# Optimization experiments

Measured on AMD Instinct MI355X. Metric: run time of the kernel, lower is better.

## Reference

```python
import jax, jax.numpy as jnp
import numpy as np

TEMPERATURE = 0.1
THRESHOLD = 0.5


def setup_inputs() -> dict:
    key = jax.random.key(0)
    k1, k2 = jax.random.split(key)
    B, D, F = 4096, 512, 128
    embeddings = jax.random.normal(k1, (B, D), dtype=jnp.float32)
    similarity_features = jax.random.normal(k2, (B, F), dtype=jnp.float32)
    return {"embeddings": embeddings, "similarity_features": similarity_features}


def reference(embeddings, similarity_features):
    B = embeddings.shape[0]
    # L2-normalize similarity features (F.normalize, eps=1e-12)
    norm = jnp.linalg.norm(similarity_features, axis=1, keepdims=True)
    f = similarity_features / jnp.maximum(norm, 1e-12)
    target_similarity = f @ f.T                                    # [B,B]
    S = (embeddings @ embeddings.T) / TEMPERATURE                  # [B,B] logits

    eye = jnp.eye(B, dtype=bool)
    offdiag = ~eye
    pos = (target_similarity > THRESHOLD) & offdiag
    neg = offdiag & ~pos

    # Per row i: logits = cat(pos_scores, neg_scores) covers ALL off-diagonal
    # entries (len = B-1), labels = 1 on positives, 0 on negatives. Mean BCE:
    #   (1/(B-1)) * sum_{j!=i} [ softplus(-S_ij) if pos else softplus(S_ij) ]
    bce = jnp.where(pos, jax.nn.softplus(-S), jax.nn.softplus(S))
    row_loss = jnp.sum(jnp.where(offdiag, bce, 0.0), axis=1) / jnp.float32(B - 1)

    # Row counted only if it has >=1 positive AND >=1 negative off-diagonal
    valid = (pos.sum(axis=1) > 0) & (neg.sum(axis=1) > 0)
    num_valid = jnp.maximum(valid.sum(), 1).astype(row_loss.dtype)
    loss = jnp.sum(jnp.where(valid, row_loss, 0.0)) / num_valid
    return loss
```

## Files before the change

kernel.cpp:

```cpp
#include <hip/hip_runtime.h>
#include <math.h>


constexpr int Bn = 4096;
constexpr int Dd = 512;
constexpr int Ff = 128;
constexpr float MARGIN = 0.015625f;

typedef __attribute__((ext_vector_type(8))) short bf16x8;
typedef __attribute__((ext_vector_type(4))) float f32x4;

__device__ __forceinline__ ushort f32_to_bf16(float x) {
    unsigned u = __float_as_uint(x);
    unsigned r = (u + 0x7FFFu + ((u >> 16) & 1u)) >> 16;
    return (ushort)r;
}
__device__ __forceinline__ float bf16_to_f32(ushort h) {
    return __uint_as_float(((unsigned)h) << 16);
}

__global__ __launch_bounds__(256) void prep_kernel(const float* __restrict__ sf,
                                                   ushort* __restrict__ fh,
                                                   ushort* __restrict__ fl,
                                                   float* __restrict__ row_sum,
                                                   int* __restrict__ pos_cnt) {
    int gid = blockIdx.x * 256 + threadIdx.x;
    if (gid < Bn) { row_sum[gid] = 0.0f; pos_cnt[gid] = 0; }

    int row = blockIdx.x * 4 + (threadIdx.x >> 6);
    int lane = threadIdx.x & 63;
    const float2 v = *reinterpret_cast<const float2*>(&sf[(size_t)row * Ff + lane * 2]);
    float ss = v.x * v.x + v.y * v.y;
    #pragma unroll
    for (int off = 32; off; off >>= 1) ss += __shfl_xor(ss, off, 64);
    float inv = 1.0f / fmaxf(sqrtf(ss), 1e-12f);
    float fx = v.x * inv, fy = v.y * inv;
    ushort hx = f32_to_bf16(fx), hy = f32_to_bf16(fy);
    ushort lx = f32_to_bf16(fx - bf16_to_f32(hx));
    ushort ly = f32_to_bf16(fy - bf16_to_f32(hy));
    ushort2 h; h.x = hx; h.y = hy;
    ushort2 l; l.x = lx; l.y = ly;
    *reinterpret_cast<ushort2*>(&fh[(size_t)row * Ff + lane * 2]) = h;
    *reinterpret_cast<ushort2*>(&fl[(size_t)row * Ff + lane * 2]) = l;
}

__device__ __forceinline__ void tri_decode(int p, int& bi, int& bj) {
    bi = (int)((sqrtf(8.0f * (float)p + 1.0f) - 1.0f) * 0.5f);
    while ((bi + 1) * (bi + 2) / 2 <= p) ++bi;
    while (bi * (bi + 1) / 2 > p) --bi;
    bj = p - bi * (bi + 1) / 2;
}

__device__ __forceinline__ void stage_tile(const ushort* __restrict__ src, int stride,
                                           int k0, char* tile, int wave, int lane) {
    #pragma unroll
    for (int q = 0; q < 4; ++q) {
        int boff = wave * 4096 + q * 1024 + lane * 16;
        int row = boff >> 7;
        int cb = (boff & 127) ^ ((row & 7) << 4);
        const ushort* g = src + (size_t)row * stride + k0 + (cb >> 1);
        __builtin_amdgcn_global_load_lds(
            (const __attribute__((address_space(1))) void*)g,
            (__attribute__((address_space(3))) void*)(tile + wave * 4096 + q * 1024),
            16, 0, 0);
    }
}

__device__ __forceinline__ void mfma_step(f32x4 (&acc)[4][4], const char* At, const char* Bt,
                                          int wrow, int wcol, int lane) {
    #pragma unroll
    for (int ks = 0; ks < 2; ++ks) {
        bf16x8 a[4], b[4];
        int koff = ks * 64 + ((lane >> 4) << 4);
        #pragma unroll
        for (int m = 0; m < 4; ++m) {
            int row = wrow + m * 16 + (lane & 15);
            a[m] = *reinterpret_cast<const bf16x8*>(At + row * 128 + (koff ^ ((row & 7) << 4)));
        }
        #pragma unroll
        for (int n = 0; n < 4; ++n) {
            int row = wcol + n * 16 + (lane & 15);
            b[n] = *reinterpret_cast<const bf16x8*>(Bt + row * 128 + (koff ^ ((row & 7) << 4)));
        }
        #pragma unroll
        for (int m = 0; m < 4; ++m)
            #pragma unroll
            for (int n = 0; n < 4; ++n)
                acc[m][n] = __builtin_amdgcn_mfma_f32_16x16x32_bf16(a[m], b[n], acc[m][n], 0, 0, 0);
    }
}

__global__ __launch_bounds__(256) void t_kernel(const ushort* __restrict__ Fh,
                                                const ushort* __restrict__ Fl,
                                                unsigned long long* __restrict__ posbits,
                                                int* __restrict__ pos_cnt) {
    __shared__ __align__(16) char smem[32768];
    __shared__ int nf;
    char* At = smem;
    char* Bt = smem + 16384;

    int bi, bj; tri_decode(blockIdx.x, bi, bj);
    const int ti = bi * 128, tj = bj * 128;
    const int tid = threadIdx.x;
    const int lane = tid & 63;
    const int wave = tid >> 6;
    const int wrow = (wave >> 1) * 64;
    const int wcol = (wave & 1) * 64;

    if (tid == 0) nf = 0;

    f32x4 acc[4][4];
    const f32x4 z4 = {0.0f, 0.0f, 0.0f, 0.0f};
    #pragma unroll
    for (int m = 0; m < 4; ++m)
        #pragma unroll
        for (int n = 0; n < 4; ++n) acc[m][n] = z4;

    for (int k0 = 0; k0 < Ff; k0 += 64) {
        stage_tile(Fh + (size_t)ti * Ff, Ff, k0, At, wave, lane);
        stage_tile(Fh + (size_t)tj * Ff, Ff, k0, Bt, wave, lane);
        __syncthreads();
        mfma_step(acc, At, Bt, wrow, wcol, lane);
        __syncthreads();
    }

    bool nr = false;
    #pragma unroll
    for (int m = 0; m < 4; ++m)
        #pragma unroll
        for (int n = 0; n < 4; ++n)
            #pragma unroll
            for (int r = 0; r < 4; ++r)
                nr |= fabsf(acc[m][n][r] - 0.5f) < MARGIN;
    if (__any(nr)) { if (lane == 0) nf = 1; }
    __syncthreads();

    if (nf) {
        for (int k0 = 0; k0 < Ff; k0 += 64) {
            stage_tile(Fh + (size_t)ti * Ff, Ff, k0, At, wave, lane);
            stage_tile(Fl + (size_t)tj * Ff, Ff, k0, Bt, wave, lane);
            __syncthreads();
            mfma_step(acc, At, Bt, wrow, wcol, lane);
            __syncthreads();
        }
        for (int k0 = 0; k0 < Ff; k0 += 64) {
            stage_tile(Fl + (size_t)ti * Ff, Ff, k0, At, wave, lane);
            stage_tile(Fh + (size_t)tj * Ff, Ff, k0, Bt, wave, lane);
            __syncthreads();
            mfma_step(acc, At, Bt, wrow, wcol, lane);
            __syncthreads();
        }
    }

    unsigned long long pm = 0;
    #pragma unroll
    for (int m = 0; m < 4; ++m)
        #pragma unroll
        for (int n = 0; n < 4; ++n)
            #pragma unroll
            for (int r = 0; r < 4; ++r)
                if (acc[m][n][r] > 0.5f) pm |= 1ull << (m * 16 + n * 4 + r);
    posbits[(size_t)blockIdx.x * 256 + tid] = pm;

    int colC[4] = {0, 0, 0, 0};
    #pragma unroll
    for (int m = 0; m < 4; ++m) {
        #pragma unroll
        for (int r = 0; r < 4; ++r) {
            int c = 0;
            int gi = ti + wrow + m * 16 + ((lane >> 4) << 2) + r;
            #pragma unroll
            for (int n = 0; n < 4; ++n) {
                int gj = tj + wcol + n * 16 + (lane & 15);
                bool pos = (pm >> (m * 16 + n * 4 + r)) & 1;
                if (gi != gj && pos) {
                    c += 1;
                    if (bi != bj) colC[n] += 1;
                }
            }
            #pragma unroll
            for (int off = 8; off; off >>= 1) c += __shfl_xor(c, off, 16);
            if ((lane & 15) == 0 && c) atomicAdd(&pos_cnt[gi], c);
        }
    }
    if (bi != bj) {
        #pragma unroll
        for (int n = 0; n < 4; ++n) {
            int c = colC[n];
            c += __shfl_xor(c, 16, 64);
            c += __shfl_xor(c, 32, 64);
            if ((lane >> 4) == 0 && c) {
                int gj = tj + wcol + n * 16 + (lane & 15);
                atomicAdd(&pos_cnt[gj], c);
            }
        }
    }
}

__global__ __launch_bounds__(256) void split_E_kernel(const float* __restrict__ E,
                                                      ushort* __restrict__ eh,
                                                      ushort* __restrict__ el,
                                                      const int* __restrict__ pos_cnt) {
    __shared__ int go;
    if (threadIdx.x == 0) go = 0;
    __syncthreads();
    bool val = false;
    for (int r = threadIdx.x; r < Bn; r += 256) {
        int pc = pos_cnt[r];
        val |= (pc > 0) && (pc < Bn - 1);
    }
    if (__any(val)) { if ((threadIdx.x & 63) == 0) go = 1; }
    __syncthreads();
    if (!go) return;

    int base = blockIdx.x * 256 + threadIdx.x;
    #pragma unroll
    for (int it = 0; it < 4; ++it) {
        size_t i = ((size_t)base + (size_t)it * 131072) * 4;
        float4 v = *reinterpret_cast<const float4*>(&E[i]);
        float c[4] = {v.x, v.y, v.z, v.w};
        ushort4 h, l;
        ushort hu[4], lu[4];
        #pragma unroll
        for (int j = 0; j < 4; ++j) {
            hu[j] = f32_to_bf16(c[j]);
            lu[j] = f32_to_bf16(c[j] - bf16_to_f32(hu[j]));
        }
        h.x = hu[0]; h.y = hu[1]; h.z = hu[2]; h.w = hu[3];
        l.x = lu[0]; l.y = lu[1]; l.z = lu[2]; l.w = lu[3];
        *reinterpret_cast<ushort4*>(&eh[i]) = h;
        *reinterpret_cast<ushort4*>(&el[i]) = l;
    }
}

__global__ __launch_bounds__(256) void s_kernel(const ushort* __restrict__ Eh,
                                                const ushort* __restrict__ El,
                                                const unsigned long long* __restrict__ posbits,
                                                const int* __restrict__ pos_cnt,
                                                float* __restrict__ row_sum) {
    __shared__ __align__(16) char smem[65536];
    __shared__ int go;
    int bi, bj; tri_decode(blockIdx.x, bi, bj);
    const int ti = bi * 128, tj = bj * 128;
    const int tid = threadIdx.x;

    if (tid == 0) go = 0;
    __syncthreads();
    int pc = (tid < 128) ? pos_cnt[ti + tid] : pos_cnt[tj + tid - 128];
    bool val = (pc > 0) && (pc < Bn - 1);
    if (__any(val)) { if ((tid & 63) == 0) go = 1; }
    __syncthreads();
    if (!go) return;

    char* Ah = smem;
    char* Al = smem + 16384;
    char* Bh = smem + 32768;
    char* Bl = smem + 49152;

    const int lane = tid & 63;
    const int wave = tid >> 6;
    const int wrow = (wave >> 1) * 64;
    const int wcol = (wave & 1) * 64;

    f32x4 acc[4][4];
    const f32x4 z4 = {0.0f, 0.0f, 0.0f, 0.0f};
    #pragma unroll
    for (int m = 0; m < 4; ++m)
        #pragma unroll
        for (int n = 0; n < 4; ++n) acc[m][n] = z4;

    for (int k0 = 0; k0 < Dd; k0 += 64) {
        stage_tile(Eh + (size_t)ti * Dd, Dd, k0, Ah, wave, lane);
        stage_tile(El + (size_t)ti * Dd, Dd, k0, Al, wave, lane);
        stage_tile(Eh + (size_t)tj * Dd, Dd, k0, Bh, wave, lane);
        stage_tile(El + (size_t)tj * Dd, Dd, k0, Bl, wave, lane);
        __syncthreads();
        mfma_step(acc, Ah, Bh, wrow, wcol, lane);
        mfma_step(acc, Ah, Bl, wrow, wcol, lane);
        mfma_step(acc, Al, Bh, wrow, wcol, lane);
        __syncthreads();
    }

    unsigned long long pm = posbits[(size_t)blockIdx.x * 256 + tid];

    float colS[4] = {0, 0, 0, 0};
    #pragma unroll
    for (int m = 0; m < 4; ++m) {
        #pragma unroll
        for (int r = 0; r < 4; ++r) {
            float s = 0.0f;
            int gi = ti + wrow + m * 16 + ((lane >> 4) << 2) + r;
            #pragma unroll
            for (int n = 0; n < 4; ++n) {
                int gj = tj + wcol + n * 16 + (lane & 15);
                if (gi != gj) {
                    float S = acc[m][n][r] * 10.0f;
                    bool pos = (pm >> (m * 16 + n * 4 + r)) & 1;
                    float x = pos ? -S : S;
                    float sp = fmaxf(x, 0.0f) + log1pf(expf(-fabsf(x)));
                    s += sp;
                    if (bi != bj) colS[n] += sp;
                }
            }
            #pragma unroll
            for (int off = 8; off; off >>= 1) s += __shfl_xor(s, off, 16);
            if ((lane & 15) == 0) atomicAdd(&row_sum[gi], s);
        }
    }
    if (bi != bj) {
        #pragma unroll
        for (int n = 0; n < 4; ++n) {
            float s = colS[n];
            s += __shfl_xor(s, 16, 64);
            s += __shfl_xor(s, 32, 64);
            if ((lane >> 4) == 0) {
                int gj = tj + wcol + n * 16 + (lane & 15);
                atomicAdd(&row_sum[gj], s);
            }
        }
    }
}

__global__ __launch_bounds__(256) void finalize_kernel(const float* __restrict__ row_sum,
                                                       const int* __restrict__ pos_cnt,
                                                       float* __restrict__ out) {
    __shared__ float ssum[256];
    __shared__ int scnt[256];
    float ls = 0.0f;
    int lc = 0;
    for (int r = threadIdx.x; r < Bn; r += 256) {
        int pz = pos_cnt[r];
        if (pz > 0 && pz < Bn - 1) {
            ls += row_sum[r] / (float)(Bn - 1);
            lc += 1;
        }
    }
    ssum[threadIdx.x] = ls;
    scnt[threadIdx.x] = lc;
    __syncthreads();
    for (int s = 128; s; s >>= 1) {
        if (threadIdx.x < s) {
            ssum[threadIdx.x] += ssum[threadIdx.x + s];
            scnt[threadIdx.x] += scnt[threadIdx.x + s];
        }
        __syncthreads();
    }
    if (threadIdx.x == 0) {
        float nv = fmaxf((float)scnt[0], 1.0f);
        out[0] = ssum[0] / nv;
    }
}

extern "C" void kernel_launch(void* const* d_in, const int* in_sizes, int n_in,
                              void* d_out, int out_size, void* d_ws, size_t ws_size,
                              hipStream_t stream) {
    const float* E = (const float*)d_in[0];
    const float* SF = (const float*)d_in[1];
    float* out = (float*)d_out;

    constexpr int NT = (Bn / 128) * (Bn / 128 + 1) / 2;

    ushort* eh = (ushort*)d_ws;
    ushort* el = eh + (size_t)Bn * Dd;
    ushort* fh = el + (size_t)Bn * Dd;
    ushort* fl = fh + (size_t)Bn * Ff;
    float* row_sum = (float*)(fl + (size_t)Bn * Ff);
    int* pos_cnt = (int*)(row_sum + Bn);
    unsigned long long* posbits = (unsigned long long*)(((size_t)(pos_cnt + Bn) + 15) & ~15ull);

    prep_kernel<<<Bn / 4, 256, 0, stream>>>(SF, fh, fl, row_sum, pos_cnt);
    t_kernel<<<NT, 256, 0, stream>>>(fh, fl, posbits, pos_cnt);
    split_E_kernel<<<512, 256, 0, stream>>>(E, eh, el, pos_cnt);
    s_kernel<<<NT, 256, 0, stream>>>(eh, el, posbits, pos_cnt, row_sum);
    finalize_kernel<<<1, 256, 0, stream>>>(row_sum, pos_cnt, out);
}
```

Measured before the change: 83.03 us.

## Fuse five kernels into one cooperative persistent kernel with grid syncs

Replaces the five separate launches (prep, T-tile, split_E, S-tile, finalize) with a single cooperative mega-kernel of 512 persistent blocks. The blocks loop over the triangular tiles and use grid.sync between phases. This removes per-launch overhead and inter-kernel gaps. In exchange it adds grid-wide barriers, limits the persistent grid to what fits two blocks per CU with 64KB LDS, and makes the finalize step run on a single block while the others idle.

```diff
diff --git a/kernel.cpp b/kernel.cpp
--- a/kernel.cpp
+++ b/kernel.cpp
@@ -1,10 +1,14 @@
 #include <hip/hip_runtime.h>
+#include <hip/hip_cooperative_groups.h>
 #include <math.h>
+
+namespace cg = cooperative_groups;
 
 
 constexpr int Bn = 4096;
 constexpr int Dd = 512;
 constexpr int Ff = 128;
+constexpr int NT = (Bn / 128) * (Bn / 128 + 1) / 2;
 constexpr float MARGIN = 0.015625f;
 
 typedef __attribute__((ext_vector_type(8))) short bf16x8;
@@ -17,31 +21,6 @@
 }
 __device__ __forceinline__ float bf16_to_f32(ushort h) {
     return __uint_as_float(((unsigned)h) << 16);
-}
-
-__global__ __launch_bounds__(256) void prep_kernel(const float* __restrict__ sf,
-                                                   ushort* __restrict__ fh,
-                                                   ushort* __restrict__ fl,
-                                                   float* __restrict__ row_sum,
-                                                   int* __restrict__ pos_cnt) {
-    int gid = blockIdx.x * 256 + threadIdx.x;
-    if (gid < Bn) { row_sum[gid] = 0.0f; pos_cnt[gid] = 0; }
-
-    int row = blockIdx.x * 4 + (threadIdx.x >> 6);
-    int lane = threadIdx.x & 63;
-    const float2 v = *reinterpret_cast<const float2*>(&sf[(size_t)row * Ff + lane * 2]);
-    float ss = v.x * v.x + v.y * v.y;
-    #pragma unroll
-    for (int off = 32; off; off >>= 1) ss += __shfl_xor(ss, off, 64);
-    float inv = 1.0f / fmaxf(sqrtf(ss), 1e-12f);
-    float fx = v.x * inv, fy = v.y * inv;
-    ushort hx = f32_to_bf16(fx), hy = f32_to_bf16(fy);
-    ushort lx = f32_to_bf16(fx - bf16_to_f32(hx));
-    ushort ly = f32_to_bf16(fy - bf16_to_f32(hy));
-    ushort2 h; h.x = hx; h.y = hy;
-    ushort2 l; l.x = lx; l.y = ly;
-    *reinterpret_cast<ushort2*>(&fh[(size_t)row * Ff + lane * 2]) = h;
-    *reinterpret_cast<ushort2*>(&fl[(size_t)row * Ff + lane * 2]) = l;
 }
 
 __device__ __forceinline__ void tri_decode(int p, int& bi, int& bj) {
@@ -90,264 +69,274 @@
     }
 }
 
-__global__ __launch_bounds__(256) void t_kernel(const ushort* __restrict__ Fh,
-                                                const ushort* __restrict__ Fl,
-                                                unsigned long long* __restrict__ posbits,
-                                                int* __restrict__ pos_cnt) {
-    __shared__ __align__(16) char smem[32768];
-    __shared__ int nf;
-    char* At = smem;
-    char* Bt = smem + 16384;
-
-    int bi, bj; tri_decode(blockIdx.x, bi, bj);
-    const int ti = bi * 128, tj = bj * 128;
+__global__ __launch_bounds__(256, 2) void mega_kernel(
+    const float* __restrict__ E, const float* __restrict__ SF,
+    ushort* __restrict__ eh, ushort* __restrict__ el,
+    ushort* __restrict__ fh, ushort* __restrict__ fl,
+    float* __restrict__ row_sum, int* __restrict__ pos_cnt,
+    int* __restrict__ any_valid, unsigned long long* __restrict__ posbits,
+    float* __restrict__ out) {
+    cg::grid_group grid = cg::this_grid();
+    __shared__ __align__(16) char smem[65536];
+    __shared__ int flagS;
     const int tid = threadIdx.x;
+    const int bid = blockIdx.x;
+    const int nb = gridDim.x;
     const int lane = tid & 63;
     const int wave = tid >> 6;
-    const int wrow = (wave >> 1) * 64;
-    const int wcol = (wave & 1) * 64;
-
-    if (tid == 0) nf = 0;
-
-    f32x4 acc[4][4];
     const f32x4 z4 = {0.0f, 0.0f, 0.0f, 0.0f};
-    #pragma unroll
-    for (int m = 0; m < 4; ++m)
-        #pragma unroll
-        for (int n = 0; n < 4; ++n) acc[m][n] = z4;
-
-    for (int k0 = 0; k0 < Ff; k0 += 64) {
-        stage_tile(Fh + (size_t)ti * Ff, Ff, k0, At, wave, lane);
-        stage_tile(Fh + (size_t)tj * Ff, Ff, k0, Bt, wave, lane);
+
+    for (int r = bid * 256 + tid; r < Bn; r += nb * 256) { row_sum[r] = 0.0f; pos_cnt[r] = 0; }
+    if (bid == 0 && tid == 0) *any_valid = 0;
+    for (int row = bid * 4 + wave; row < Bn; row += nb * 4) {
+        float2 v = *reinterpret_cast<const float2*>(&SF[(size_t)row * Ff + lane * 2]);
+        float ss = v.x * v.x + v.y * v.y;
+        #pragma unroll
+        for (int off = 32; off; off >>= 1) ss += __shfl_xor(ss, off, 64);
+        float inv = 1.0f / fmaxf(sqrtf(ss), 1e-12f);
+        float fx = v.x * inv, fy = v.y * inv;
+        ushort hx = f32_to_bf16(fx), hy = f32_to_bf16(fy);
+        ushort lx = f32_to_bf16(fx - bf16_to_f32(hx));
+        ushort ly = f32_to_bf16(fy - bf16_to_f32(hy));
+        ushort2 h; h.x = hx; h.y = hy;
+        ushort2 l; l.x = lx; l.y = ly;
+        *reinterpret_cast<ushort2*>(&fh[(size_t)row * Ff + lane * 2]) = h;
+        *reinterpret_cast<ushort2*>(&fl[(size_t)row * Ff + lane * 2]) = l;
+    }
+    grid.sync();
+
+    for (int p = bid; p < NT; p += nb) {
         __syncthreads();
-        mfma_step(acc, At, Bt, wrow, wcol, lane);
+        if (tid == 0) flagS = 0;
+        int bi, bj; tri_decode(p, bi, bj);
+        const int ti = bi * 128, tj = bj * 128;
+        const int wrow = (wave >> 1) * 64;
+        const int wcol = (wave & 1) * 64;
+        char* At = smem;
+        char* Bt = smem + 16384;
+
+        f32x4 acc[4][4];
+        #pragma unroll
+        for (int m = 0; m < 4; ++m)
+            #pragma unroll
+            for (int n = 0; n < 4; ++n) acc[m][n] = z4;
+
+        for (int k0 = 0; k0 < Ff; k0 += 64) {
+            stage_tile(fh + (size_t)ti * Ff, Ff, k0, At, wave, lane);
+            stage_tile(fh + (size_t)tj * Ff, Ff, k0, Bt, wave, lane);
+            __syncthreads();
+            mfma_step(acc, At, Bt, wrow, wcol, lane);
+            __syncthreads();
+        }
+
+        bool nr = false;
+        #pragma unroll
+        for (int m = 0; m < 4; ++m)
+            #pragma unroll
+            for (int n = 0; n < 4; ++n)
+                #pragma unroll
+                for (int r = 0; r < 4; ++r)
+                    nr |= fabsf(acc[m][n][r] - 0.5f) < MARGIN;
+        if (__any(nr)) { if (lane == 0) flagS = 1; }
         __syncthreads();
-    }
-
-    bool nr = false;
-    #pragma unroll
-    for (int m = 0; m < 4; ++m)
-        #pragma unroll
-        for (int n = 0; n < 4; ++n)
-            #pragma unroll
-            for (int r = 0; r < 4; ++r)
-                nr |= fabsf(acc[m][n][r] - 0.5f) < MARGIN;
-    if (__any(nr)) { if (lane == 0) nf = 1; }
-    __syncthreads();
-
-    if (nf) {
-        for (int k0 = 0; k0 < Ff; k0 += 64) {
-            stage_tile(Fh + (size_t)ti * Ff, Ff, k0, At, wave, lane);
-            stage_tile(Fl + (size_t)tj * Ff, Ff, k0, Bt, wave, lane);
-            __syncthreads();
-            mfma_step(acc, At, Bt, wrow, wcol, lane);
-            __syncthreads();
-        }
-        for (int k0 = 0; k0 < Ff; k0 += 64) {
-            stage_tile(Fl + (size_t)ti * Ff, Ff, k0, At, wave, lane);
-            stage_tile(Fh + (size_t)tj * Ff, Ff, k0, Bt, wave, lane);
-            __syncthreads();
-            mfma_step(acc, At, Bt, wrow, wcol, lane);
-            __syncthreads();
-        }
-    }
-
-    unsigned long long pm = 0;
-    #pragma unroll
-    for (int m = 0; m < 4; ++m)
-        #pragma unroll
-        for (int n = 0; n < 4; ++n)
-            #pragma unroll
-            for (int r = 0; r < 4; ++r)
-                if (acc[m][n][r] > 0.5f) pm |= 1ull << (m * 16 + n * 4 + r);
-    posbits[(size_t)blockIdx.x * 256 + tid] = pm;
-
-    int colC[4] = {0, 0, 0, 0};
-    #pragma unroll
-    for (int m = 0; m < 4; ++m) {
-        #pragma unroll
-        for (int r = 0; r < 4; ++r) {
-            int c = 0;
-            int gi = ti + wrow + m * 16 + ((lane >> 4) << 2) + r;
+
+        if (flagS) {
+            for (int k0 = 0; k0 < Ff; k0 += 64) {
+                stage_tile(fh + (size_t)ti * Ff, Ff, k0, At, wave, lane);
+                stage_tile(fl + (size_t)tj * Ff, Ff, k0, Bt, wave, lane);
+                __syncthreads();
+                mfma_step(acc, At, Bt, wrow, wcol, lane);
+                __syncthreads();
+            }
+            for (int k0 = 0; k0 < Ff; k0 += 64) {
+                stage_tile(fl + (size_t)ti * Ff, Ff, k0, At, wave, lane);
+                stage_tile(fh + (size_t)tj * Ff, Ff, k0, Bt, wave, lane);
+                __syncthreads();
+                mfma_step(acc, At, Bt, wrow, wcol, lane);
+                __syncthreads();
+            }
+        }
+
+        unsigned long long pm = 0;
+        #pragma unroll
+        for (int m = 0; m < 4; ++m)
+            #pragma unroll
+            for (int n = 0; n < 4; ++n)
+                #pragma unroll
+                for (int r = 0; r < 4; ++r)
+                    if (acc[m][n][r] > 0.5f) pm |= 1ull << (m * 16 + n * 4 + r);
+        posbits[(size_t)p * 256 + tid] = pm;
+
+        int colC[4] = {0, 0, 0, 0};
+        #pragma unroll
+        for (int m = 0; m < 4; ++m) {
+            #pragma unroll
+            for (int r = 0; r < 4; ++r) {
+                int c = 0;
+                int gi = ti + wrow + m * 16 + ((lane >> 4) << 2) + r;
+                #pragma unroll
+                for (int n = 0; n < 4; ++n) {
+                    int gj = tj + wcol + n * 16 + (lane & 15);
+                    bool pos = (pm >> (m * 16 + n * 4 + r)) & 1;
+                    if (gi != gj && pos) {
+                        c += 1;
+                        if (bi != bj) colC[n] += 1;
+                    }
+                }
+                #pragma unroll
+                for (int off = 8; off; off >>= 1) c += __shfl_xor(c, off, 16);
+                if ((lane & 15) == 0 && c) atomicAdd(&pos_cnt[gi], c);
+            }
+        }
+        if (bi != bj) {
             #pragma unroll
             for (int n = 0; n < 4; ++n) {
-                int gj = tj + wcol + n * 16 + (lane & 15);
-                bool pos = (pm >> (m * 16 + n * 4 + r)) & 1;
-                if (gi != gj && pos) {
-                    c += 1;
-                    if (bi != bj) colC[n] += 1;
+                int c = colC[n];
+                c += __shfl_xor(c, 16, 64);
+                c += __shfl_xor(c, 32, 64);
+                if ((lane >> 4) == 0 && c) {
+                    int gj = tj + wcol + n * 16 + (lane & 15);
+                    atomicAdd(&pos_cnt[gj], c);
                 }
             }
-            #pragma unroll
-            for (int off = 8; off; off >>= 1) c += __shfl_xor(c, off, 16);
-            if ((lane & 15) == 0 && c) atomicAdd(&pos_cnt[gi], c);
-        }
-    }
-    if (bi != bj) {
-        #pragma unroll
-        for (int n = 0; n < 4; ++n) {
-            int c = colC[n];
-            c += __shfl_xor(c, 16, 64);
-            c += __shfl_xor(c, 32, 64);
-            if ((lane >> 4) == 0 && c) {
-                int gj = tj + wcol + n * 16 + (lane & 15);
-                atomicAdd(&pos_cnt[gj], c);
-            }
-        }
-    }
-}
-
-__global__ __launch_bounds__(256) void split_E_kernel(const float* __restrict__ E,
-                                                      ushort* __restrict__ eh,
-                                                      ushort* __restrict__ el,
-                                                      const int* __restrict__ pos_cnt) {
-    __shared__ int go;
-    if (threadIdx.x == 0) go = 0;
-    __syncthreads();
-    bool val = false;
-    for (int r = threadIdx.x; r < Bn; r += 256) {
-        int pc = pos_cnt[r];
-        val |= (pc > 0) && (pc < Bn - 1);
-    }
-    if (__any(val)) { if ((threadIdx.x & 63) == 0) go = 1; }
-    __syncthreads();
-    if (!go) return;
-
-    int base = blockIdx.x * 256 + threadIdx.x;
-    #pragma unroll
-    for (int it = 0; it < 4; ++it) {
-        size_t i = ((size_t)base + (size_t)it * 131072) * 4;
-        float4 v = *reinterpret_cast<const float4*>(&E[i]);
-        float c[4] = {v.x, v.y, v.z, v.w};
-        ushort4 h, l;
-        ushort hu[4], lu[4];
-        #pragma unroll
-        for (int j = 0; j < 4; ++j) {
-            hu[j] = f32_to_bf16(c[j]);
-            lu[j] = f32_to_bf16(c[j] - bf16_to_f32(hu[j]));
-        }
-        h.x = hu[0]; h.y = hu[1]; h.z = hu[2]; h.w = hu[3];
-        l.x = lu[0]; l.y = lu[1]; l.z = lu[2]; l.w = lu[3];
-        *reinterpret_cast<ushort4*>(&eh[i]) = h;
-        *reinterpret_cast<ushort4*>(&el[i]) = l;
-    }
-}
-
-__global__ __launch_bounds__(256) void s_kernel(const ushort* __restrict__ Eh,
-                                                const ushort* __restrict__ El,
-                                                const unsigned long long* __restrict__ posbits,
-                                                const int* __restrict__ pos_cnt,
-                                                float* __restrict__ row_sum) {
-    __shared__ __align__(16) char smem[65536];
-    __shared__ int go;
-    int bi, bj; tri_decode(blockIdx.x, bi, bj);
-    const int ti = bi * 128, tj = bj * 128;
-    const int tid = threadIdx.x;
-
-    if (tid == 0) go = 0;
-    __syncthreads();
-    int pc = (tid < 128) ? pos_cnt[ti + tid] : pos_cnt[tj + tid - 128];
-    bool val = (pc > 0) && (pc < Bn - 1);
-    if (__any(val)) { if ((tid & 63) == 0) go = 1; }
-    __syncthreads();
-    if (!go) return;
-
-    char* Ah = smem;
-    char* Al = smem + 16384;
-    char* Bh = smem + 32768;
-    char* Bl = smem + 49152;
-
-    const int lane = tid & 63;
-    const int wave = tid >> 6;
-    const int wrow = (wave >> 1) * 64;
-    const int wcol = (wave & 1) * 64;
-
-    f32x4 acc[4][4];
-    const f32x4 z4 = {0.0f, 0.0f, 0.0f, 0.0f};
-    #pragma unroll
-    for (int m = 0; m < 4; ++m)
-        #pragma unroll
-        for (int n = 0; n < 4; ++n) acc[m][n] = z4;
-
-    for (int k0 = 0; k0 < Dd; k0 += 64) {
-        stage_tile(Eh + (size_t)ti * Dd, Dd, k0, Ah, wave, lane);
-        stage_tile(El + (size_t)ti * Dd, Dd, k0, Al, wave, lane);
-        stage_tile(Eh + (size_t)tj * Dd, Dd, k0, Bh, wave, lane);
-        stage_tile(El + (size_t)tj * Dd, Dd, k0, Bl, wave, lane);
+        }
+    }
+    grid.sync();
+
+    {
+        bool val = false;
+        for (int r = bid * 256 + tid; r < Bn; r += nb * 256) {
+            int pc = pos_cnt[r];
+            val |= (pc > 0) && (pc < Bn - 1);
+        }
+        if (__any(val)) { if (lane == 0) atomicOr(any_valid, 1); }
+    }
+    grid.sync();
+
+    int av = *any_valid;
+    if (av) {
+        for (int idx = bid * 256 + tid; idx < Bn * Dd / 4; idx += nb * 256) {
+            size_t i = (size_t)idx * 4;
+            float4 v = *reinterpret_cast<const float4*>(&E[i]);
+            float c[4] = {v.x, v.y, v.z, v.w};
+            ushort4 h, l;
+            ushort hu[4], lu[4];
+            #pragma unroll
+            for (int j = 0; j < 4; ++j) {
+                hu[j] = f32_to_bf16(c[j]);
+                lu[j] = f32_to_bf16(c[j] - bf16_to_f32(hu[j]));
+            }
+            h.x = hu[0]; h.y = hu[1]; h.z = hu[2]; h.w = hu[3];
+            l.x = lu[0]; l.y = lu[1]; l.z = lu[2]; l.w = lu[3];
+            *reinterpret_cast<ushort4*>(&eh[i]) = h;
+            *reinterpret_cast<ushort4*>(&el[i]) = l;
+        }
+        grid.sync();
+
+        for (int p = bid; p < NT; p += nb) {
+            __syncthreads();
+            if (tid == 0) flagS = 0;
+            int bi, bj; tri_decode(p, bi, bj);
+            const int ti = bi * 128, tj = bj * 128;
+            __syncthreads();
+            int pc = (tid < 128) ? pos_cnt[ti + tid] : pos_cnt[tj + tid - 128];
+            bool val = (pc > 0) && (pc < Bn - 1);
+            if (__any(val)) { if (lane == 0) flagS = 1; }
+            __syncthreads();
+            if (!flagS) continue;
+
+            char* Ah = smem;
+            char* Al = smem + 16384;
+            char* Bh = smem + 32768;
+            char* Bl = smem + 49152;
+            const int wrow = (wave >> 1) * 64;
+            const int wcol = (wave & 1) * 64;
+
+            f32x4 acc[4][4];
+            #pragma unroll
+            for (int m = 0; m < 4; ++m)
+                #pragma unroll
+                for (int n = 0; n < 4; ++n) acc[m][n] = z4;
+
+            for (int k0 = 0; k0 < Dd; k0 += 64) {
+                stage_tile(eh + (size_t)ti * Dd, Dd, k0, Ah, wave, lane);
+                stage_tile(el + (size_t)ti * Dd, Dd, k0, Al, wave, lane);
+                stage_tile(eh + (size_t)tj * Dd, Dd, k0, Bh, wave, lane);
+                stage_tile(el + (size_t)tj * Dd, Dd, k0, Bl, wave, lane);
+                __syncthreads();
+                mfma_step(acc, Ah, Bh, wrow, wcol, lane);
+                mfma_step(acc, Ah, Bl, wrow, wcol, lane);
+                mfma_step(acc, Al, Bh, wrow, wcol, lane);
+                __syncthreads();
+            }
+
+            unsigned long long pm = posbits[(size_t)p * 256 + tid];
+            float colS[4] = {0, 0, 0, 0};
+            #pragma unroll
+            for (int m = 0; m < 4; ++m) {
+                #pragma unroll
+                for (int r = 0; r < 4; ++r) {
+                    float s = 0.0f;
+                    int gi = ti + wrow + m * 16 + ((lane >> 4) << 2) + r;
+                    #pragma unroll
+                    for (int n = 0; n < 4; ++n) {
+                        int gj = tj + wcol + n * 16 + (lane & 15);
+                        if (gi != gj) {
+                            float S = acc[m][n][r] * 10.0f;
+                            bool pos = (pm >> (m * 16 + n * 4 + r)) & 1;
+                            float x = pos ? -S : S;
+                            float sp = fmaxf(x, 0.0f) + log1pf(expf(-fabsf(x)));
+                            s += sp;
+                            if (bi != bj) colS[n] += sp;
+                        }
+                    }
+                    #pragma unroll
+                    for (int off = 8; off; off >>= 1) s += __shfl_xor(s, off, 16);
+                    if ((lane & 15) == 0) atomicAdd(&row_sum[gi], s);
+                }
+            }
+            if (bi != bj) {
+                #pragma unroll
+                for (int n = 0; n < 4; ++n) {
+                    float s = colS[n];
+                    s += __shfl_xor(s, 16, 64);
+                    s += __shfl_xor(s, 32, 64);
+                    if ((lane >> 4) == 0) {
+                        int gj = tj + wcol + n * 16 + (lane & 15);
+                        atomicAdd(&row_sum[gj], s);
+                    }
+                }
+            }
+        }
+        grid.sync();
+    }
+
+    if (bid == 0) {
+        float* ssum = (float*)smem;
+        int* scnt = (int*)(smem + 1024);
+        float ls = 0.0f;
+        int lc = 0;
+        for (int r = tid; r < Bn; r += 256) {
+            int pz = pos_cnt[r];
+            if (pz > 0 && pz < Bn - 1) {
+                ls += row_sum[r] / (float)(Bn - 1);
+                lc += 1;
+            }
+        }
+        ssum[tid] = ls;
+        scnt[tid] = lc;
         __syncthreads();
-        mfma_step(acc, Ah, Bh, wrow, wcol, lane);
-        mfma_step(acc, Ah, Bl, wrow, wcol, lane);
-        mfma_step(acc, Al, Bh, wrow, wcol, lane);
-        __syncthreads();
-    }
-
-    unsigned long long pm = posbits[(size_t)blockIdx.x * 256 + tid];
-
-    float colS[4] = {0, 0, 0, 0};
-    #pragma unroll
-    for (int m = 0; m < 4; ++m) {
-        #pragma unroll
-        for (int r = 0; r < 4; ++r) {
-            float s = 0.0f;
-            int gi = ti + wrow + m * 16 + ((lane >> 4) << 2) + r;
-            #pragma unroll
-            for (int n = 0; n < 4; ++n) {
-                int gj = tj + wcol + n * 16 + (lane & 15);
-                if (gi != gj) {
-                    float S = acc[m][n][r] * 10.0f;
-                    bool pos = (pm >> (m * 16 + n * 4 + r)) & 1;
-                    float x = pos ? -S : S;
-                    float sp = fmaxf(x, 0.0f) + log1pf(expf(-fabsf(x)));
-                    s += sp;
-                    if (bi != bj) colS[n] += sp;
-                }
-            }
-            #pragma unroll
-            for (int off = 8; off; off >>= 1) s += __shfl_xor(s, off, 16);
-            if ((lane & 15) == 0) atomicAdd(&row_sum[gi], s);
-        }
-    }
-    if (bi != bj) {
-        #pragma unroll
-        for (int n = 0; n < 4; ++n) {
-            float s = colS[n];
-            s += __shfl_xor(s, 16, 64);
-            s += __shfl_xor(s, 32, 64);
-            if ((lane >> 4) == 0) {
-                int gj = tj + wcol + n * 16 + (lane & 15);
-                atomicAdd(&row_sum[gj], s);
-            }
-        }
-    }
-}
-
-__global__ __launch_bounds__(256) void finalize_kernel(const float* __restrict__ row_sum,
-                                                       const int* __restrict__ pos_cnt,
-                                                       float* __restrict__ out) {
-    __shared__ float ssum[256];
-    __shared__ int scnt[256];
-    float ls = 0.0f;
-    int lc = 0;
-    for (int r = threadIdx.x; r < Bn; r += 256) {
-        int pz = pos_cnt[r];
-        if (pz > 0 && pz < Bn - 1) {
-            ls += row_sum[r] / (float)(Bn - 1);
-            lc += 1;
-        }
-    }
-    ssum[threadIdx.x] = ls;
-    scnt[threadIdx.x] = lc;
-    __syncthreads();
-    for (int s = 128; s; s >>= 1) {
-        if (threadIdx.x < s) {
-            ssum[threadIdx.x] += ssum[threadIdx.x + s];
-            scnt[threadIdx.x] += scnt[threadIdx.x + s];
-        }
-        __syncthreads();
-    }
-    if (threadIdx.x == 0) {
-        float nv = fmaxf((float)scnt[0], 1.0f);
-        out[0] = ssum[0] / nv;
+        for (int s = 128; s; s >>= 1) {
+            if (tid < s) {
+                ssum[tid] += ssum[tid + s];
+                scnt[tid] += scnt[tid + s];
+            }
+            __syncthreads();
+        }
+        if (tid == 0) {
+            float nv = fmaxf((float)scnt[0], 1.0f);
+            out[0] = ssum[0] / nv;
+        }
     }
 }
 
@@ -358,19 +347,21 @@
     const float* SF = (const float*)d_in[1];
     float* out = (float*)d_out;
 
-    constexpr int NT = (Bn / 128) * (Bn / 128 + 1) / 2;
-
     ushort* eh = (ushort*)d_ws;
     ushort* el = eh + (size_t)Bn * Dd;
     ushort* fh = el + (size_t)Bn * Dd;
     ushort* fl = fh + (size_t)Bn * Ff;
     float* row_sum = (float*)(fl + (size_t)Bn * Ff);
     int* pos_cnt = (int*)(row_sum + Bn);
-    unsigned long long* posbits = (unsigned long long*)(((size_t)(pos_cnt + Bn) + 15) & ~15ull);
-
-    prep_kernel<<<Bn / 4, 256, 0, stream>>>(SF, fh, fl, row_sum, pos_cnt);
-    t_kernel<<<NT, 256, 0, stream>>>(fh, fl, posbits, pos_cnt);
-    split_E_kernel<<<512, 256, 0, stream>>>(E, eh, el, pos_cnt);
-    s_kernel<<<NT, 256, 0, stream>>>(eh, el, posbits, pos_cnt, row_sum);
-    finalize_kernel<<<1, 256, 0, stream>>>(row_sum, pos_cnt, out);
-}
+    int* any_valid = pos_cnt + Bn;
+    unsigned long long* posbits =
+        (unsigned long long*)(((size_t)(any_valid + 16) + 15) & ~15ull);
+
+    constexpr int GRID = 512;
+
+    void* args[] = {(void*)&E, (void*)&SF, (void*)&eh, (void*)&el,
+                    (void*)&fh, (void*)&fl, (void*)&row_sum, (void*)&pos_cnt,
+                    (void*)&any_valid, (void*)&posbits, (void*)&out};
+    hipLaunchCooperativeKernel((void*)mega_kernel, dim3(GRID), dim3(256),
+                               args, 0, stream);
+}
```

New measurement: 231.2 us. +178.5%, slower.

## Fuse feature normalization and E bf16 splitting into tile GEMM kernels

Applied to the files above, without the earlier changes.

Removes the prep and split_E kernels. The t kernel now normalizes features and converts them to bf16 on the fly into LDS, and the s kernel converts fp32 embeddings into hi/lo bf16 tiles while staging them. Positive counts move from global atomics to per-block LDS counts written into a per-row-block count array, which later kernels sum. This cuts launches and intermediate global traffic, but each tile now redoes normalization and conversion work and loses the async global_load_lds path.

```diff
diff --git a/kernel.cpp b/kernel.cpp
--- a/kernel.cpp
+++ b/kernel.cpp
@@ -5,6 +5,8 @@
 constexpr int Bn = 4096;
 constexpr int Dd = 512;
 constexpr int Ff = 128;
+constexpr int NB = Bn / 128;
+constexpr int NT = NB * (NB + 1) / 2;
 constexpr float MARGIN = 0.015625f;
 
 typedef __attribute__((ext_vector_type(8))) short bf16x8;
@@ -17,31 +19,6 @@
 }
 __device__ __forceinline__ float bf16_to_f32(ushort h) {
     return __uint_as_float(((unsigned)h) << 16);
-}
-
-__global__ __launch_bounds__(256) void prep_kernel(const float* __restrict__ sf,
-                                                   ushort* __restrict__ fh,
-                                                   ushort* __restrict__ fl,
-                                                   float* __restrict__ row_sum,
-                                                   int* __restrict__ pos_cnt) {
-    int gid = blockIdx.x * 256 + threadIdx.x;
-    if (gid < Bn) { row_sum[gid] = 0.0f; pos_cnt[gid] = 0; }
-
-    int row = blockIdx.x * 4 + (threadIdx.x >> 6);
-    int lane = threadIdx.x & 63;
-    const float2 v = *reinterpret_cast<const float2*>(&sf[(size_t)row * Ff + lane * 2]);
-    float ss = v.x * v.x + v.y * v.y;
-    #pragma unroll
-    for (int off = 32; off; off >>= 1) ss += __shfl_xor(ss, off, 64);
-    float inv = 1.0f / fmaxf(sqrtf(ss), 1e-12f);
-    float fx = v.x * inv, fy = v.y * inv;
-    ushort hx = f32_to_bf16(fx), hy = f32_to_bf16(fy);
-    ushort lx = f32_to_bf16(fx - bf16_to_f32(hx));
-    ushort ly = f32_to_bf16(fy - bf16_to_f32(hy));
-    ushort2 h; h.x = hx; h.y = hy;
-    ushort2 l; l.x = lx; l.y = ly;
-    *reinterpret_cast<ushort2*>(&fh[(size_t)row * Ff + lane * 2]) = h;
-    *reinterpret_cast<ushort2*>(&fl[(size_t)row * Ff + lane * 2]) = l;
 }
 
 __device__ __forceinline__ void tri_decode(int p, int& bi, int& bj) {
@@ -51,217 +28,207 @@
     bj = p - bi * (bi + 1) / 2;
 }
 
-__device__ __forceinline__ void stage_tile(const ushort* __restrict__ src, int stride,
-                                           int k0, char* tile, int wave, int lane) {
+__device__ __forceinline__ void mfma_step(f32x4 (&acc)[4][4], const char* At, const char* Bt,
+                                          int wrow, int wcol, int lane) {
+    #pragma unroll
+    for (int ks = 0; ks < 2; ++ks) {
+        bf16x8 a[4], b[4];
+        int koff = ks * 64 + ((lane >> 4) << 4);
+        #pragma unroll
+        for (int m = 0; m < 4; ++m) {
+            int row = wrow + m * 16 + (lane & 15);
+            a[m] = *reinterpret_cast<const bf16x8*>(At + row * 128 + (koff ^ ((row & 7) << 4)));
+        }
+        #pragma unroll
+        for (int n = 0; n < 4; ++n) {
+            int row = wcol + n * 16 + (lane & 15);
+            b[n] = *reinterpret_cast<const bf16x8*>(Bt + row * 128 + (koff ^ ((row & 7) << 4)));
+        }
+        #pragma unroll
+        for (int m = 0; m < 4; ++m)
+            #pragma unroll
+            for (int n = 0; n < 4; ++n)
+                acc[m][n] = __builtin_amdgcn_mfma_f32_16x16x32_bf16(a[m], b[n], acc[m][n], 0, 0, 0);
+    }
+}
+
+__device__ __forceinline__ void norm_stage(const float* __restrict__ SF, int rowBase,
+                                           bool lo, char* buf, int wave, int lane) {
+    #pragma unroll 4
+    for (int i = 0; i < 32; ++i) {
+        int lr = wave * 32 + i;
+        float2 v = *reinterpret_cast<const float2*>(&SF[(size_t)(rowBase + lr) * Ff + lane * 2]);
+        float ss = v.x * v.x + v.y * v.y;
+        #pragma unroll
+        for (int off = 32; off; off >>= 1) ss += __shfl_xor(ss, off, 64);
+        float inv = 1.0f / fmaxf(sqrtf(ss), 1e-12f);
+        float fx = v.x * inv, fy = v.y * inv;
+        ushort hx = f32_to_bf16(fx), hy = f32_to_bf16(fy);
+        ushort ox = hx, oy = hy;
+        if (lo) {
+            ox = f32_to_bf16(fx - bf16_to_f32(hx));
+            oy = f32_to_bf16(fy - bf16_to_f32(hy));
+        }
+        int cb = (4 * lane) & 127;
+        int d = cb ^ ((lr & 7) << 4);
+        ushort2 o; o.x = ox; o.y = oy;
+        *reinterpret_cast<ushort2*>(buf + (lane >> 5) * 16384 + lr * 128 + d) = o;
+    }
+}
+
+__global__ __launch_bounds__(256, 2) void t_fused_kernel(
+    const float* __restrict__ SF, unsigned long long* __restrict__ posbits,
+    int* __restrict__ cnt, float* __restrict__ row_sum) {
+    __shared__ __align__(16) char smem[65536];
+    __shared__ int flagS;
+    __shared__ int rowCnt[128];
+    __shared__ int colCnt[128];
+
+    const int tid = threadIdx.x;
+    const int lane = tid & 63;
+    const int wave = tid >> 6;
+
+    if (blockIdx.x < 16) row_sum[blockIdx.x * 256 + tid] = 0.0f;
+    if (tid == 0) flagS = 0;
+
+    int bi, bj; tri_decode(blockIdx.x, bi, bj);
+    const int ti = bi * 128, tj = bj * 128;
+    const int wrow = (wave >> 1) * 64;
+    const int wcol = (wave & 1) * 64;
+    char* Abuf = smem;
+    char* Bbuf = smem + 32768;
+
+    f32x4 acc[4][4];
+    const f32x4 z4 = {0.0f, 0.0f, 0.0f, 0.0f};
+    #pragma unroll
+    for (int m = 0; m < 4; ++m)
+        #pragma unroll
+        for (int n = 0; n < 4; ++n) acc[m][n] = z4;
+
+    norm_stage(SF, ti, false, Abuf, wave, lane);
+    norm_stage(SF, tj, false, Bbuf, wave, lane);
+    __syncthreads();
+    mfma_step(acc, Abuf, Bbuf, wrow, wcol, lane);
+    mfma_step(acc, Abuf + 16384, Bbuf + 16384, wrow, wcol, lane);
+
+    bool nr = false;
+    #pragma unroll
+    for (int m = 0; m < 4; ++m)
+        #pragma unroll
+        for (int n = 0; n < 4; ++n)
+            #pragma unroll
+            for (int r = 0; r < 4; ++r)
+                nr |= fabsf(acc[m][n][r] - 0.5f) < MARGIN;
+    if (__any(nr)) { if (lane == 0) flagS = 1; }
+    __syncthreads();
+
+    if (flagS) {
+        norm_stage(SF, tj, true, Bbuf, wave, lane);
+        __syncthreads();
+        mfma_step(acc, Abuf, Bbuf, wrow, wcol, lane);
+        mfma_step(acc, Abuf + 16384, Bbuf + 16384, wrow, wcol, lane);
+        __syncthreads();
+        norm_stage(SF, ti, true, Abuf, wave, lane);
+        norm_stage(SF, tj, false, Bbuf, wave, lane);
+        __syncthreads();
+        mfma_step(acc, Abuf, Bbuf, wrow, wcol, lane);
+        mfma_step(acc, Abuf + 16384, Bbuf + 16384, wrow, wcol, lane);
+    }
+
+    unsigned long long pm = 0;
+    #pragma unroll
+    for (int m = 0; m < 4; ++m)
+        #pragma unroll
+        for (int n = 0; n < 4; ++n)
+            #pragma unroll
+            for (int r = 0; r < 4; ++r)
+                if (acc[m][n][r] > 0.5f) pm |= 1ull << (m * 16 + n * 4 + r);
+    posbits[(size_t)blockIdx.x * 256 + tid] = pm;
+
+    if (tid < 128) rowCnt[tid] = 0; else colCnt[tid - 128] = 0;
+    __syncthreads();
+    #pragma unroll
+    for (int m = 0; m < 4; ++m) {
+        #pragma unroll
+        for (int r = 0; r < 4; ++r) {
+            int lrow = wrow + m * 16 + ((lane >> 4) << 2) + r;
+            int gi = ti + lrow;
+            #pragma unroll
+            for (int n = 0; n < 4; ++n) {
+                int lcol = wcol + n * 16 + (lane & 15);
+                int gj = tj + lcol;
+                if (gi != gj && ((pm >> (m * 16 + n * 4 + r)) & 1)) {
+                    atomicAdd(&rowCnt[lrow], 1);
+                    atomicAdd(&colCnt[lcol], 1);
+                }
+            }
+        }
+    }
+    __syncthreads();
+    if (tid < 128) cnt[(size_t)(ti + tid) * NB + bj] = rowCnt[tid];
+    else if (bi != bj) cnt[(size_t)(tj + tid - 128) * NB + bi] = colCnt[tid - 128];
+}
+
+__device__ __forceinline__ void stage_conv(const float* __restrict__ E, int rowBase,
+                                           int k0, char* Hbuf, char* Lbuf,
+                                           int wave, int lane) {
     #pragma unroll
     for (int q = 0; q < 4; ++q) {
         int boff = wave * 4096 + q * 1024 + lane * 16;
         int row = boff >> 7;
-        int cb = (boff & 127) ^ ((row & 7) << 4);
-        const ushort* g = src + (size_t)row * stride + k0 + (cb >> 1);
-        __builtin_amdgcn_global_load_lds(
-            (const __attribute__((address_space(1))) void*)g,
-            (__attribute__((address_space(3))) void*)(tile + wave * 4096 + q * 1024),
-            16, 0, 0);
-    }
-}
-
-__device__ __forceinline__ void mfma_step(f32x4 (&acc)[4][4], const char* At, const char* Bt,
-                                          int wrow, int wcol, int lane) {
-    #pragma unroll
-    for (int ks = 0; ks < 2; ++ks) {
-        bf16x8 a[4], b[4];
-        int koff = ks * 64 + ((lane >> 4) << 4);
-        #pragma unroll
-        for (int m = 0; m < 4; ++m) {
-            int row = wrow + m * 16 + (lane & 15);
-            a[m] = *reinterpret_cast<const bf16x8*>(At + row * 128 + (koff ^ ((row & 7) << 4)));
-        }
-        #pragma unroll
-        for (int n = 0; n < 4; ++n) {
-            int row = wcol + n * 16 + (lane & 15);
-            b[n] = *reinterpret_cast<const bf16x8*>(Bt + row * 128 + (koff ^ ((row & 7) << 4)));
-        }
-        #pragma unroll
-        for (int m = 0; m < 4; ++m)
-            #pragma unroll
-            for (int n = 0; n < 4; ++n)
-                acc[m][n] = __builtin_amdgcn_mfma_f32_16x16x32_bf16(a[m], b[n], acc[m][n], 0, 0, 0);
-    }
-}
-
-__global__ __launch_bounds__(256) void t_kernel(const ushort* __restrict__ Fh,
-                                                const ushort* __restrict__ Fl,
-                                                unsigned long long* __restrict__ posbits,
-                                                int* __restrict__ pos_cnt) {
-    __shared__ __align__(16) char smem[32768];
-    __shared__ int nf;
-    char* At = smem;
-    char* Bt = smem + 16384;
-
+        int d = boff & 127;
+        int cb = d ^ ((row & 7) << 4);
+        const float* src = &E[(size_t)(rowBase + row) * Dd + k0 + (cb >> 1)];
+        float4 v0 = *reinterpret_cast<const float4*>(src);
+        float4 v1 = *reinterpret_cast<const float4*>(src + 4);
+        float c[8] = {v0.x, v0.y, v0.z, v0.w, v1.x, v1.y, v1.z, v1.w};
+        bf16x8 hv, lv;
+        #pragma unroll
+        for (int j = 0; j < 8; ++j) {
+            ushort h = f32_to_bf16(c[j]);
+            hv[j] = (short)h;
+            lv[j] = (short)f32_to_bf16(c[j] - bf16_to_f32(h));
+        }
+        *reinterpret_cast<bf16x8*>(Hbuf + boff) = hv;
+        *reinterpret_cast<bf16x8*>(Lbuf + boff) = lv;
+    }
+}
+
+__global__ __launch_bounds__(256, 2) void s_kernel(
+    const float* __restrict__ E, const unsigned long long* __restrict__ posbits,
+    const int* __restrict__ cnt, float* __restrict__ row_sum) {
+    __shared__ __align__(16) char smem[65536];
+    __shared__ int go;
+    const int tid = threadIdx.x;
     int bi, bj; tri_decode(blockIdx.x, bi, bj);
     const int ti = bi * 128, tj = bj * 128;
-    const int tid = threadIdx.x;
+
+    if (tid == 0) go = 0;
+    __syncthreads();
+    {
+        int r = (tid < 128) ? (ti + tid) : (tj + tid - 128);
+        const int4* c4 = reinterpret_cast<const int4*>(&cnt[(size_t)r * NB]);
+        int pc = 0;
+        #pragma unroll
+        for (int q = 0; q < 8; ++q) {
+            int4 v = c4[q];
+            pc += v.x + v.y + v.z + v.w;
+        }
+        bool val = (pc > 0) && (pc < Bn - 1);
+        if (__any(val)) { if ((tid & 63) == 0) go = 1; }
+    }
+    __syncthreads();
+    if (!go) return;
+
     const int lane = tid & 63;
     const int wave = tid >> 6;
     const int wrow = (wave >> 1) * 64;
     const int wcol = (wave & 1) * 64;
-
-    if (tid == 0) nf = 0;
-
-    f32x4 acc[4][4];
-    const f32x4 z4 = {0.0f, 0.0f, 0.0f, 0.0f};
-    #pragma unroll
-    for (int m = 0; m < 4; ++m)
-        #pragma unroll
-        for (int n = 0; n < 4; ++n) acc[m][n] = z4;
-
-    for (int k0 = 0; k0 < Ff; k0 += 64) {
-        stage_tile(Fh + (size_t)ti * Ff, Ff, k0, At, wave, lane);
-        stage_tile(Fh + (size_t)tj * Ff, Ff, k0, Bt, wave, lane);
-        __syncthreads();
-        mfma_step(acc, At, Bt, wrow, wcol, lane);
-        __syncthreads();
-    }
-
-    bool nr = false;
-    #pragma unroll
-    for (int m = 0; m < 4; ++m)
-        #pragma unroll
-        for (int n = 0; n < 4; ++n)
-            #pragma unroll
-            for (int r = 0; r < 4; ++r)
-                nr |= fabsf(acc[m][n][r] - 0.5f) < MARGIN;
-    if (__any(nr)) { if (lane == 0) nf = 1; }
-    __syncthreads();
-
-    if (nf) {
-        for (int k0 = 0; k0 < Ff; k0 += 64) {
-            stage_tile(Fh + (size_t)ti * Ff, Ff, k0, At, wave, lane);
-            stage_tile(Fl + (size_t)tj * Ff, Ff, k0, Bt, wave, lane);
-            __syncthreads();
-            mfma_step(acc, At, Bt, wrow, wcol, lane);
-            __syncthreads();
-        }
-        for (int k0 = 0; k0 < Ff; k0 += 64) {
-            stage_tile(Fl + (size_t)ti * Ff, Ff, k0, At, wave, lane);
-            stage_tile(Fh + (size_t)tj * Ff, Ff, k0, Bt, wave, lane);
-            __syncthreads();
-            mfma_step(acc, At, Bt, wrow, wcol, lane);
-            __syncthreads();
-        }
-    }
-
-    unsigned long long pm = 0;
-    #pragma unroll
-    for (int m = 0; m < 4; ++m)
-        #pragma unroll
-        for (int n = 0; n < 4; ++n)
-            #pragma unroll
-            for (int r = 0; r < 4; ++r)
-                if (acc[m][n][r] > 0.5f) pm |= 1ull << (m * 16 + n * 4 + r);
-    posbits[(size_t)blockIdx.x * 256 + tid] = pm;
-
-    int colC[4] = {0, 0, 0, 0};
-    #pragma unroll
-    for (int m = 0; m < 4; ++m) {
-        #pragma unroll
-        for (int r = 0; r < 4; ++r) {
-            int c = 0;
-            int gi = ti + wrow + m * 16 + ((lane >> 4) << 2) + r;
-            #pragma unroll
-            for (int n = 0; n < 4; ++n) {
-                int gj = tj + wcol + n * 16 + (lane & 15);
-                bool pos = (pm >> (m * 16 + n * 4 + r)) & 1;
-                if (gi != gj && pos) {
-                    c += 1;
-                    if (bi != bj) colC[n] += 1;
-                }
-            }
-            #pragma unroll
-            for (int off = 8; off; off >>= 1) c += __shfl_xor(c, off, 16);
-            if ((lane & 15) == 0 && c) atomicAdd(&pos_cnt[gi], c);
-        }
-    }
-    if (bi != bj) {
-        #pragma unroll
-        for (int n = 0; n < 4; ++n) {
-            int c = colC[n];
-            c += __shfl_xor(c, 16, 64);
-            c += __shfl_xor(c, 32, 64);
-            if ((lane >> 4) == 0 && c) {
-                int gj = tj + wcol + n * 16 + (lane & 15);
-                atomicAdd(&pos_cnt[gj], c);
-            }
-        }
-    }
-}
-
-__global__ __launch_bounds__(256) void split_E_kernel(const float* __restrict__ E,
-                                                      ushort* __restrict__ eh,
-                                                      ushort* __restrict__ el,
-                                                      const int* __restrict__ pos_cnt) {
-    __shared__ int go;
-    if (threadIdx.x == 0) go = 0;
-    __syncthreads();
-    bool val = false;
-    for (int r = threadIdx.x; r < Bn; r += 256) {
-        int pc = pos_cnt[r];
-        val |= (pc > 0) && (pc < Bn - 1);
-    }
-    if (__any(val)) { if ((threadIdx.x & 63) == 0) go = 1; }
-    __syncthreads();
-    if (!go) return;
-
-    int base = blockIdx.x * 256 + threadIdx.x;
-    #pragma unroll
-    for (int it = 0; it < 4; ++it) {
-        size_t i = ((size_t)base + (size_t)it * 131072) * 4;
-        float4 v = *reinterpret_cast<const float4*>(&E[i]);
-        float c[4] = {v.x, v.y, v.z, v.w};
-        ushort4 h, l;
-        ushort hu[4], lu[4];
-        #pragma unroll
-        for (int j = 0; j < 4; ++j) {
-            hu[j] = f32_to_bf16(c[j]);
-            lu[j] = f32_to_bf16(c[j] - bf16_to_f32(hu[j]));
-        }
-        h.x = hu[0]; h.y = hu[1]; h.z = hu[2]; h.w = hu[3];
-        l.x = lu[0]; l.y = lu[1]; l.z = lu[2]; l.w = lu[3];
-        *reinterpret_cast<ushort4*>(&eh[i]) = h;
-        *reinterpret_cast<ushort4*>(&el[i]) = l;
-    }
-}
-
-__global__ __launch_bounds__(256) void s_kernel(const ushort* __restrict__ Eh,
-                                                const ushort* __restrict__ El,
-                                                const unsigned long long* __restrict__ posbits,
-                                                const int* __restrict__ pos_cnt,
-                                                float* __restrict__ row_sum) {
-    __shared__ __align__(16) char smem[65536];
-    __shared__ int go;
-    int bi, bj; tri_decode(blockIdx.x, bi, bj);
-    const int ti = bi * 128, tj = bj * 128;
-    const int tid = threadIdx.x;
-
-    if (tid == 0) go = 0;
-    __syncthreads();
-    int pc = (tid < 128) ? pos_cnt[ti + tid] : pos_cnt[tj + tid - 128];
-    bool val = (pc > 0) && (pc < Bn - 1);
-    if (__any(val)) { if ((tid & 63) == 0) go = 1; }
-    __syncthreads();
-    if (!go) return;
-
     char* Ah = smem;
     char* Al = smem + 16384;
     char* Bh = smem + 32768;
     char* Bl = smem + 49152;
 
-    const int lane = tid & 63;
-    const int wave = tid >> 6;
-    const int wrow = (wave >> 1) * 64;
-    const int wcol = (wave & 1) * 64;
-
     f32x4 acc[4][4];
     const f32x4 z4 = {0.0f, 0.0f, 0.0f, 0.0f};
     #pragma unroll
@@ -270,19 +237,16 @@
         for (int n = 0; n < 4; ++n) acc[m][n] = z4;
 
     for (int k0 = 0; k0 < Dd; k0 += 64) {
-        stage_tile(Eh + (size_t)ti * Dd, Dd, k0, Ah, wave, lane);
-        stage_tile(El + (size_t)ti * Dd, Dd, k0, Al, wave, lane);
-        stage_tile(Eh + (size_t)tj * Dd, Dd, k0, Bh, wave, lane);
-        stage_tile(El + (size_t)tj * Dd, Dd, k0, Bl, wave, lane);
+        __syncthreads();
+        stage_conv(E, ti, k0, Ah, Al, wave, lane);
+        stage_conv(E, tj, k0, Bh, Bl, wave, lane);
         __syncthreads();
         mfma_step(acc, Ah, Bh, wrow, wcol, lane);
         mfma_step(acc, Ah, Bl, wrow, wcol, lane);
         mfma_step(acc, Al, Bh, wrow, wcol, lane);
-        __syncthreads();
     }
 
     unsigned long long pm = posbits[(size_t)blockIdx.x * 256 + tid];
-
     float colS[4] = {0, 0, 0, 0};
     #pragma unroll
     for (int m = 0; m < 4; ++m) {
@@ -321,16 +285,22 @@
     }
 }
 
-__global__ __launch_bounds__(256) void finalize_kernel(const float* __restrict__ row_sum,
-                                                       const int* __restrict__ pos_cnt,
-                                                       float* __restrict__ out) {
+__global__ __launch_bounds__(256) void finalize_kernel(
+    const float* __restrict__ row_sum, const int* __restrict__ cnt,
+    float* __restrict__ out) {
     __shared__ float ssum[256];
     __shared__ int scnt[256];
     float ls = 0.0f;
     int lc = 0;
     for (int r = threadIdx.x; r < Bn; r += 256) {
-        int pz = pos_cnt[r];
-        if (pz > 0 && pz < Bn - 1) {
+        const int4* c4 = reinterpret_cast<const int4*>(&cnt[(size_t)r * NB]);
+        int pc = 0;
+        #pragma unroll
+        for (int q = 0; q < 8; ++q) {
+            int4 v = c4[q];
+            pc += v.x + v.y + v.z + v.w;
+        }
+        if (pc > 0 && pc < Bn - 1) {
             ls += row_sum[r] / (float)(Bn - 1);
             lc += 1;
         }
@@ -358,19 +328,12 @@
     const float* SF = (const float*)d_in[1];
     float* out = (float*)d_out;
 
-    constexpr int NT = (Bn / 128) * (Bn / 128 + 1) / 2;
-
-    ushort* eh = (ushort*)d_ws;
-    ushort* el = eh + (size_t)Bn * Dd;
-    ushort* fh = el + (size_t)Bn * Dd;
-    ushort* fl = fh + (size_t)Bn * Ff;
-    float* row_sum = (float*)(fl + (size_t)Bn * Ff);
-    int* pos_cnt = (int*)(row_sum + Bn);
-    unsigned long long* posbits = (unsigned long long*)(((size_t)(pos_cnt + Bn) + 15) & ~15ull);
-
-    prep_kernel<<<Bn / 4, 256, 0, stream>>>(SF, fh, fl, row_sum, pos_cnt);
-    t_kernel<<<NT, 256, 0, stream>>>(fh, fl, posbits, pos_cnt);
-    split_E_kernel<<<512, 256, 0, stream>>>(E, eh, el, pos_cnt);
-    s_kernel<<<NT, 256, 0, stream>>>(eh, el, posbits, pos_cnt, row_sum);
-    finalize_kernel<<<1, 256, 0, stream>>>(row_sum, pos_cnt, out);
-}
+    int* cnt = (int*)d_ws;
+    float* row_sum = (float*)(cnt + (size_t)Bn * NB);
+    unsigned long long* posbits =
+        (unsigned long long*)(((size_t)(row_sum + Bn) + 15) & ~15ull);
+
+    t_fused_kernel<<<NT, 256, 0, stream>>>(SF, posbits, cnt, row_sum);
+    s_kernel<<<NT, 256, 0, stream>>>(E, posbits, cnt, row_sum);
+    finalize_kernel<<<1, 256, 0, stream>>>(row_sum, cnt, out);
+}
```

After: 109.1 us. 31.4% more time.
